# Kernel tuning notes

Hardware: AMD Instinct MI355X
Metric: run time of the kernel (lower is better)

The kernel has to match this reference:

```python
import jax, jax.numpy as jnp
import numpy as np

T, D, N, K, V = 4, 1024, 256, 64, 32000
SGLD_A, SGLD_B, SGLD_C = 0.01, 1.0, 0.55
PHI_VAR, ETA_VAR = 1.0, 1.0
ZERO = 1e-6

def jax_exp(x):
    return jnp.clip(jnp.exp(jnp.clip(x, -700.0, 700.0)), ZERO)

def setup_inputs() -> dict:
    key = jax.random.key(0)
    ks = jax.random.split(key, 13)
    W = jax.random.randint(ks[0], (T, D, N), 0, V, dtype=jnp.int32)
    Z = jax.random.randint(ks[1], (T, D, N), 0, K - 1, dtype=jnp.int32)
    prop_word_idx = jax.random.randint(ks[2], (T, D, N), 0, N, dtype=jnp.int32)
    prop_topic = jax.random.randint(ks[3], (T, D, N), 0, K - 1, dtype=jnp.int32)
    u_mh = jax.random.uniform(ks[4], (T, D, N, 2), dtype=jnp.float32)
    noise_eta = jax.random.normal(ks[5], (T, D), dtype=jnp.float32)
    noise_phi = jax.random.normal(ks[6], (T,), dtype=jnp.float32)
    alpha = jax.random.normal(ks[7], (T, K), dtype=jnp.float32)
    phi = jax.random.normal(ks[8], (T, V, K), dtype=jnp.float32) * 0.1
    eta = jax.random.normal(ks[9], (T, D, K), dtype=jnp.float32) * 0.1
    CDK = jax.random.uniform(ks[10], (T, D, K), dtype=jnp.float32) * (N / K)
    CWK = jax.random.uniform(ks[11], (T, V, K), dtype=jnp.float32)
    CK = jax.random.uniform(ks[12], (T, K), dtype=jnp.float32) * (D * N / K)
    return dict(W=W, Z=Z, prop_word_idx=prop_word_idx, prop_topic=prop_topic,
                u_mh=u_mh, noise_eta=noise_eta, noise_phi=noise_phi,
                alpha=alpha, phi=phi, eta=eta, CDK=CDK, CWK=CWK, CK=CK)

def reference(W, Z, prop_word_idx, prop_topic, u_mh, noise_eta, noise_phi,
              alpha, phi, eta, CDK, CWK, CK):
    eps = SGLD_A * (SGLD_B + 0.0) ** (-SGLD_C)  # SGLD step at iteration 0

    # --- SGLD update of eta (per doc), vmapped over (T, D) via broadcasting ---
    prior_eta = (alpha[:, None, :] - eta) / ETA_VAR                 # [T,D,K]
    grad_eta = CDK - N * jax.nn.softmax(eta, axis=-1)               # [T,D,K]
    eta_new = eta + eps / 2 * (grad_eta + prior_eta) + noise_eta[..., None] * eps

    tt = jnp.arange(T)[:, None, None]   # [T,1,1]
    dd = jnp.arange(D)[None, :, None]   # [1,D,1]

    # --- MH step 1: word-proposal (acceptance via phi ratio) ---
    pre = Z                                                           # [T,D,N]
    prop1 = jnp.take_along_axis(Z, prop_word_idx, axis=2)             # [T,D,N]
    a1 = jax_exp(phi[tt, W, prop1]) / jax_exp(phi[tt, W, pre])
    k1 = jnp.where(u_mh[..., 0] < a1, prop1, pre)

    # --- MH step 2: topic-proposal (acceptance via eta ratio) ---
    a2 = jax_exp(eta_new[tt, dd, prop_topic]) / jax_exp(eta_new[tt, dd, k1])
    z_new = jnp.where(u_mh[..., 1] < a2, prop_topic, k1)              # [T,D,N]

    # --- scatter counter updates (add new assignment, remove old) ---
    CDK_new = CDK.at[tt, dd, z_new].add(1.0).at[tt, dd, Z].add(-1.0)
    CWK_new = CWK.at[tt, W, z_new].add(1.0).at[tt, W, Z].add(-1.0)
    CK_new = CK.at[tt, z_new].add(1.0).at[tt, Z].add(-1.0)

    # --- SGLD update of phi: sequential over T (reads updated phi[t-1]) ---
    rows = [phi[t] for t in range(T)]   # each [V,K]
    phi_sigma = 1.0 / (1.0 / 100.0 + 1.0 / PHI_VAR)
    for t in range(T):
        if t == 0:
            prior = (2.0 * phi[1] * (phi_sigma / PHI_VAR) - 2.0 * rows[0]) / PHI_VAR
        elif t == T - 1:
            prior = (rows[t - 1] - rows[t]) / PHI_VAR
        else:
            prior = (phi[t + 1] + rows[t - 1] - 2.0 * rows[t]) / PHI_VAR
        grad = CWK_new[t] - CK_new[t][None, :] * jax.nn.softmax(rows[t], axis=0)
        rows[t] = rows[t] + eps / 2 * (grad + prior) + noise_phi[t] * eps
    phi_new = jnp.stack(rows)

    return (eta_new, phi_new, CDK_new, CWK_new, CK_new, z_new)
```

## Files before the change

kernel.cpp:

```cpp
#include <hip/hip_runtime.h>

#define T 4
#define D 1024
#define NN 256
#define K 64
#define V 32000
#define VK (V*K)
#define TD (T*D)
#define CAP 4096

__device__ __forceinline__ float jexp(float x) {
    x = fminf(fmaxf(x, -700.0f), 700.0f);
    return fmaxf(expf(x), 1e-6f);
}


__global__ void fused_kernel(const int* __restrict__ W, const int* __restrict__ Z,
                             const int* __restrict__ pwi, const int* __restrict__ ptop,
                             const float* __restrict__ u, const float* __restrict__ phi,
                             const float* __restrict__ eta,
                             const float* __restrict__ alpha,
                             const float* __restrict__ noise_eta,
                             const float* __restrict__ CDK,
                             const float* __restrict__ CK,
                             float* __restrict__ S_part,
                             float* __restrict__ CK_new,
                             float* __restrict__ eta_new,
                             float* __restrict__ CDK_new,
                             unsigned int* __restrict__ resv,
                             unsigned int* __restrict__ list,
                             float* __restrict__ z_out)
{
    int blk = blockIdx.x;
    int n = threadIdx.x;

    __shared__ float sm[256];
    __shared__ float esh[K];
    __shared__ int   hist[K];
    __shared__ int   bcnt[8];
    __shared__ int   bbase[8];

    if (blk < 500) {
        if (blk == 0) CK_new[n] = CK[n];
        int t = blk / 125;
        int vbase = (blk % 125) * 256;
        int k = n & 63;
        int rr = n >> 6;
        const float* base = phi + (size_t)t * VK;
        float s = 0.0f;
        #pragma unroll 4
        for (int it = 0; it < 64; ++it) {
            int v = vbase + it * 4 + rr;
            s += expf(base[v * K + k]);
        }
        sm[n] = s;
        __syncthreads();
        if (n < 64) {
            S_part[blk * 64 + n] = sm[n] + sm[n + 64] +
                                   sm[n + 128] + sm[n + 192];
        }
        return;
    }

    int b = blk - 500;
    int r = ((b & 7) << 9) | (b >> 3);
    int t = r >> 10;
    int slice = (b >> 3) & 15;

    int w     = W[r * NN + n];
    int pre   = Z[r * NN + n];
    int pw    = pwi[r * NN + n];
    int prop1 = Z[r * NN + pw];
    int pt    = ptop[r * NN + n];
    float2 uu = ((const float2*)u)[(size_t)r * NN + n];

    const float* prow = phi + ((size_t)t * V + w) * K;
    float f1 = prow[prop1];
    float f0 = prow[pre];

    float cdk = 0.0f;
    if (n < 64) {
        float x = eta[r * K + n];
        float m = x;
        #pragma unroll
        for (int off = 32; off >= 1; off >>= 1)
            m = fmaxf(m, __shfl_xor(m, off, 64));
        float e = expf(x - m);
        float s = e;
        #pragma unroll
        for (int off = 32; off >= 1; off >>= 1)
            s += __shfl_xor(s, off, 64);
        float smx = e / s;
        cdk = CDK[r * K + n];
        float grad  = cdk - (float)NN * smx;
        float prior = alpha[t * K + n] - x;
        float en = x + 0.005f * (grad + prior) + noise_eta[r] * 0.01f;
        esh[n] = en;
        eta_new[r * K + n] = en;
    } else if (n < 128) {
        hist[n - 64] = 0;
    } else if (n < 136) {
        bcnt[n - 128] = 0;
    }
    __syncthreads();

    float a1 = jexp(f1) / jexp(f0);
    int k1 = (uu.x < a1) ? prop1 : pre;

    float a2 = jexp(esh[pt]) / jexp(esh[k1]);
    int z = (uu.y < a2) ? pt : k1;

    atomicAdd(&hist[z], 1);
    atomicAdd(&hist[pre], -1);

    int keep = (z != pre);
    int bucket = w / 4000;
    int myidx = 0;
    if (keep) myidx = atomicAdd(&bcnt[bucket], 1);
    __syncthreads();

    if (n < 8) {
        bbase[n] = (int)atomicAdd(&resv[(t * 8 + n) * 16 + slice],
                                  (unsigned int)bcnt[n]);
    }
    __syncthreads();

    z_out[r * NN + n] = (float)z;
    if (keep) {
        int slot = bbase[bucket] + myidx;
        if (slot < CAP) {
            unsigned int pk = (unsigned int)w | ((unsigned int)z << 15) |
                              ((unsigned int)pre << 21);
            list[(size_t)((t * 8 + bucket) * 16 + slice) * CAP + slot] = pk;
        }
    }
    if (n < K) {
        CDK_new[r * K + n] = cdk + (float)hist[n];
    }
}

__global__ void cwk_kernel(const unsigned int* __restrict__ list,
                           const unsigned int* __restrict__ resv,
                           const float* __restrict__ CWK,
                           float* __restrict__ CWK_new)
{
    int b = blockIdx.x;
    int xcd = b & 7;
    int j = b >> 3;
    int grp = j >> 5;
    int win = j & 31;
    int tb  = grp * 8 + xcd;
    int t = tb >> 3, bucket = tb & 7;
    int vbase = bucket * 4000 + win * 125;

    __shared__ unsigned int plusH[125 * 16];
    __shared__ unsigned int minusH[125 * 16];
    for (int i = threadIdx.x; i < 2000; i += 256) { plusH[i] = 0u; minusH[i] = 0u; }
    __syncthreads();

    int segbase = (t * 8 + bucket) * 16;
    for (int s = 0; s < 16; ++s) {
        int len = (int)resv[segbase + s]; if (len > CAP) len = CAP;
        const unsigned int* lp = list + (size_t)(segbase + s) * CAP;
        for (int i = threadIdx.x; i < len; i += 256) {
            unsigned int pk = lp[i];
            int wv = (int)(pk & 32767u);
            unsigned int vl = (unsigned int)(wv - vbase);
            if (vl < 125u) {
                int z  = (int)((pk >> 15) & 63u);
                int pr = (int)((pk >> 21) & 63u);
                atomicAdd(&plusH [vl * 16 + (z  >> 2)], 1u << ((z  & 3) * 8));
                atomicAdd(&minusH[vl * 16 + (pr >> 2)], 1u << ((pr & 3) * 8));
            }
        }
    }
    __syncthreads();

    const float4* src = (const float4*)(CWK     + ((size_t)t * V + vbase) * 64);
    float4*       dst = (float4*)      (CWK_new + ((size_t)t * V + vbase) * 64);
    for (int i4 = threadIdx.x; i4 < 2000; i4 += 256) {
        unsigned int pl = plusH[i4];
        unsigned int mi = minusH[i4];
        float4 c = src[i4];
        float4 o;
        #pragma unroll
        for (int jj = 0; jj < 4; ++jj) {
            int sh = jj * 8;
            (&o.x)[jj] = (&c.x)[jj] + (float)((pl >> sh) & 255u)
                                    - (float)((mi >> sh) & 255u);
        }
        dst[i4] = o;
    }
}

__global__ void reduce_kernel(const float* __restrict__ S_part,
                              const float* __restrict__ CDKn,
                              const float* __restrict__ CDK,
                              float* __restrict__ S,
                              float* __restrict__ CK_new)
{
    int b = blockIdx.x;
    int tid = threadIdx.x;

    if (b < 4 && tid < 64) {
        float s = 0.0f;
        #pragma unroll 5
        for (int i = 0; i < 125; ++i)
            s += S_part[(b * 125 + i) * 64 + tid];
        S[b * 64 + tid] = s;
    }

    int t  = b >> 4;
    int k  = tid & 63;
    int dl = tid >> 6;
    int dbase = (b & 15) << 6;
    float s = 0.0f;
    #pragma unroll
    for (int i = 0; i < 16; ++i) {
        int d = dbase + dl + (i << 2);
        size_t idx = ((size_t)(t << 10) + d) * 64 + k;
        s += CDKn[idx] - CDK[idx];
    }
    __shared__ float sm[256];
    sm[tid] = s;
    __syncthreads();
    if (tid < 64) {
        float tot = sm[k] + sm[k + 64] + sm[k + 128] + sm[k + 192];
        if (tot != 0.0f) atomicAdd(&CK_new[(t << 6) + k], tot);
    }
}

__global__ void phi_update_kernel(const float* __restrict__ phi,
                                  const float* __restrict__ CWKn,
                                  const float* __restrict__ CKn,
                                  const float* __restrict__ S,
                                  const float* __restrict__ noise_phi,
                                  float* __restrict__ phi_new)
{
    int i4 = blockIdx.x * 256 + threadIdx.x;
    int kg = i4 & 15;
    const float eps = 0.01f;
    const float half_eps = 0.005f;
    const float sig = 1.0f / 1.01f;

    const float4* phi4  = (const float4*)phi;
    const float4* cwk4  = (const float4*)CWKn;
    const float4* ck4   = (const float4*)CKn;
    const float4* s4    = (const float4*)S;
    float4*       out4  = (float4*)phi_new;

    float4 p0 = phi4[i4];
    float4 p1 = phi4[i4 +     512000];
    float4 p2 = phi4[i4 + 2 * 512000];
    float4 p3 = phi4[i4 + 3 * 512000];

    float4 c0 = cwk4[i4];
    float4 c1 = cwk4[i4 +     512000];
    float4 c2 = cwk4[i4 + 2 * 512000];
    float4 c3 = cwk4[i4 + 3 * 512000];

    float4 ckn0 = ck4[kg],      ckn1 = ck4[16 + kg];
    float4 ckn2 = ck4[32 + kg], ckn3 = ck4[48 + kg];
    float4 ss0 = s4[kg],        ss1 = s4[16 + kg];
    float4 ss2 = s4[32 + kg],   ss3 = s4[48 + kg];

    float np0 = noise_phi[0] * eps, np1 = noise_phi[1] * eps;
    float np2 = noise_phi[2] * eps, np3 = noise_phi[3] * eps;

    float4 o0, o1, o2, o3;
    #pragma unroll
    for (int j = 0; j < 4; ++j) {
        float q0 = (&p0.x)[j], q1 = (&p1.x)[j], q2 = (&p2.x)[j], q3 = (&p3.x)[j];
        float g0 = (&c0.x)[j] - (&ckn0.x)[j] * (expf(q0) / (&ss0.x)[j]);
        float g1 = (&c1.x)[j] - (&ckn1.x)[j] * (expf(q1) / (&ss1.x)[j]);
        float g2 = (&c2.x)[j] - (&ckn2.x)[j] * (expf(q2) / (&ss2.x)[j]);
        float g3 = (&c3.x)[j] - (&ckn3.x)[j] * (expf(q3) / (&ss3.x)[j]);

        float r0 = q0 + half_eps * (g0 + 2.0f * q1 * sig - 2.0f * q0) + np0;
        float r1 = q1 + half_eps * (g1 + q2 + r0 - 2.0f * q1)         + np1;
        float r2 = q2 + half_eps * (g2 + q3 + r1 - 2.0f * q2)         + np2;
        float r3 = q3 + half_eps * (g3 + r2 - q3)                      + np3;

        (&o0.x)[j] = r0; (&o1.x)[j] = r1; (&o2.x)[j] = r2; (&o3.x)[j] = r3;
    }

    out4[i4]              = o0;
    out4[i4 +     512000] = o1;
    out4[i4 + 2 * 512000] = o2;
    out4[i4 + 3 * 512000] = o3;
}

extern "C" void kernel_launch(void* const* d_in, const int* in_sizes, int n_in,
                              void* d_out, int out_size, void* d_ws, size_t ws_size,
                              hipStream_t stream)
{
    const int*   W         = (const int*)  d_in[0];
    const int*   Z         = (const int*)  d_in[1];
    const int*   pwi       = (const int*)  d_in[2];
    const int*   ptop      = (const int*)  d_in[3];
    const float* u_mh      = (const float*)d_in[4];
    const float* noise_eta = (const float*)d_in[5];
    const float* noise_phi = (const float*)d_in[6];
    const float* alpha     = (const float*)d_in[7];
    const float* phi       = (const float*)d_in[8];
    const float* eta       = (const float*)d_in[9];
    const float* CDK       = (const float*)d_in[10];
    const float* CWK       = (const float*)d_in[11];
    const float* CK        = (const float*)d_in[12];

    float* out     = (float*)d_out;
    float* eta_new = out;
    float* phi_new = out + 262144;
    float* CDK_new = out + 8454144;
    float* CWK_new = out + 8716288;
    float* CK_new  = out + 16908288;
    float* z_out   = out + 16908544;

    float* ws      = (float*)d_ws;
    float* S       = ws;
    float* S_part  = ws + 256;
    unsigned int* resv = (unsigned int*)(ws + 256 + 32000);
    unsigned int* list = resv + 512;

    hipMemsetAsync(resv, 0, 512 * sizeof(unsigned int), stream);

    fused_kernel<<<500 + TD, 256, 0, stream>>>(W, Z, pwi, ptop, u_mh, phi,
                                               eta, alpha, noise_eta, CDK, CK,
                                               S_part, CK_new,
                                               eta_new, CDK_new, resv, list, z_out);
    cwk_kernel<<<1024, 256, 0, stream>>>(list, resv, CWK, CWK_new);
    reduce_kernel<<<64, 256, 0, stream>>>(S_part, CDK_new, CDK, S, CK_new);
    phi_update_kernel<<<VK / 1024, 256, 0, stream>>>(phi, CWK_new, CK_new, S,
                                                     noise_phi, phi_new);
}
```

Baseline: 262.3 us.

## Use finer vocabulary buckets for CWK scatter lists and vectorize list decoding

Raises the number of word buckets per time step from 8 to 32, so each cwk_kernel block scans only the list entries for a 1000-word range instead of a 4000-word range. This cuts the redundant list reads and filtering done across the 32 windows. List decoding also moves to per-wave segments read as uint4. Per-segment capacity drops to 1024, which could overflow and silently drop updates if a bucket gets unusually many changed assignments.

```diff
diff --git a/kernel.cpp b/kernel.cpp
--- a/kernel.cpp
+++ b/kernel.cpp
@@ -7,7 +7,8 @@
 #define V 32000
 #define VK (V*K)
 #define TD (T*D)
-#define CAP 4096
+#define NB 32
+#define CAP 1024
 
 __device__ __forceinline__ float jexp(float x) {
     x = fminf(fmaxf(x, -700.0f), 700.0f);
@@ -37,8 +38,8 @@
     __shared__ float sm[256];
     __shared__ float esh[K];
     __shared__ int   hist[K];
-    __shared__ int   bcnt[8];
-    __shared__ int   bbase[8];
+    __shared__ int   bcnt[NB];
+    __shared__ int   bbase[NB];
 
     if (blk < 500) {
         if (blk == 0) CK_new[n] = CK[n];
@@ -99,7 +100,7 @@
         eta_new[r * K + n] = en;
     } else if (n < 128) {
         hist[n - 64] = 0;
-    } else if (n < 136) {
+    } else if (n < 128 + NB) {
         bcnt[n - 128] = 0;
     }
     __syncthreads();
@@ -114,13 +115,13 @@
     atomicAdd(&hist[pre], -1);
 
     int keep = (z != pre);
-    int bucket = w / 4000;
+    int bucket = w / 1000;
     int myidx = 0;
     if (keep) myidx = atomicAdd(&bcnt[bucket], 1);
     __syncthreads();
 
-    if (n < 8) {
-        bbase[n] = (int)atomicAdd(&resv[(t * 8 + n) * 16 + slice],
+    if (n < NB) {
+        bbase[n] = (int)atomicAdd(&resv[(t * NB + n) * 16 + slice],
                                   (unsigned int)bcnt[n]);
     }
     __syncthreads();
@@ -131,7 +132,7 @@
         if (slot < CAP) {
             unsigned int pk = (unsigned int)w | ((unsigned int)z << 15) |
                               ((unsigned int)pre << 21);
-            list[(size_t)((t * 8 + bucket) * 16 + slice) * CAP + slot] = pk;
+            list[(size_t)((t * NB + bucket) * 16 + slice) * CAP + slot] = pk;
         }
     }
     if (n < K) {
@@ -145,35 +146,45 @@
                            float* __restrict__ CWK_new)
 {
     int b = blockIdx.x;
-    int xcd = b & 7;
-    int j = b >> 3;
-    int grp = j >> 5;
-    int win = j & 31;
-    int tb  = grp * 8 + xcd;
-    int t = tb >> 3, bucket = tb & 7;
-    int vbase = bucket * 4000 + win * 125;
+    int xcd    = b & 7;
+    int tbh    = (b >> 3) & 15;
+    int window = b >> 7;
+    int tb = tbh * 8 + xcd;
+    int t = tb >> 5, bucket = tb & 31;
+    int vbase = bucket * 1000 + window * 125;
 
     __shared__ unsigned int plusH[125 * 16];
     __shared__ unsigned int minusH[125 * 16];
     for (int i = threadIdx.x; i < 2000; i += 256) { plusH[i] = 0u; minusH[i] = 0u; }
     __syncthreads();
 
-    int segbase = (t * 8 + bucket) * 16;
-    for (int s = 0; s < 16; ++s) {
+    int wave = threadIdx.x >> 6;
+    int lane = threadIdx.x & 63;
+    int segbase = tb * 16;
+
+#define DECODE(PK) {                                                        \
+        int wv = (int)((PK) & 32767u);                                      \
+        unsigned int vl = (unsigned int)(wv - vbase);                       \
+        if (vl < 125u) {                                                    \
+            int zz = (int)(((PK) >> 15) & 63u);                             \
+            int pr = (int)(((PK) >> 21) & 63u);                             \
+            atomicAdd(&plusH [vl * 16 + (zz >> 2)], 1u << ((zz & 3) * 8));  \
+            atomicAdd(&minusH[vl * 16 + (pr >> 2)], 1u << ((pr & 3) * 8));  \
+        } }
+
+    for (int s = wave; s < 16; s += 4) {
         int len = (int)resv[segbase + s]; if (len > CAP) len = CAP;
         const unsigned int* lp = list + (size_t)(segbase + s) * CAP;
-        for (int i = threadIdx.x; i < len; i += 256) {
-            unsigned int pk = lp[i];
-            int wv = (int)(pk & 32767u);
-            unsigned int vl = (unsigned int)(wv - vbase);
-            if (vl < 125u) {
-                int z  = (int)((pk >> 15) & 63u);
-                int pr = (int)((pk >> 21) & 63u);
-                atomicAdd(&plusH [vl * 16 + (z  >> 2)], 1u << ((z  & 3) * 8));
-                atomicAdd(&minusH[vl * 16 + (pr >> 2)], 1u << ((pr & 3) * 8));
-            }
-        }
-    }
+        const uint4* lp4 = (const uint4*)lp;
+        int n4 = len >> 2;
+        for (int i = lane; i < n4; i += 64) {
+            uint4 q = lp4[i];
+            DECODE(q.x); DECODE(q.y); DECODE(q.z); DECODE(q.w);
+        }
+        int base4 = n4 << 2;
+        if (lane < (len & 3)) { unsigned int pk = lp[base4 + lane]; DECODE(pk); }
+    }
+#undef DECODE
     __syncthreads();
 
     const float4* src = (const float4*)(CWK     + ((size_t)t * V + vbase) * 64);
@@ -320,9 +331,9 @@
     float* S       = ws;
     float* S_part  = ws + 256;
     unsigned int* resv = (unsigned int*)(ws + 256 + 32000);
-    unsigned int* list = resv + 512;
-
-    hipMemsetAsync(resv, 0, 512 * sizeof(unsigned int), stream);
+    unsigned int* list = resv + 2048;
+
+    hipMemsetAsync(resv, 0, 2048 * sizeof(unsigned int), stream);
 
     fused_kernel<<<500 + TD, 256, 0, stream>>>(W, Z, pwi, ptop, u_mh, phi,
                                                eta, alpha, noise_eta, CDK, CK,
```

New measurement: 224.4 us. 14.5% less time.
